# Performance work log

Measured on AMD Instinct MI355X. Metric: run time of the kernel, lower is better.

## Reference

```python
import jax, jax.numpy as jnp
import numpy as np

L, B, D_MODEL, N_STATE = 512, 32, 256, 16
DT_RANK = 16          # ceil(d_model / 16)
D_INNER = D_MODEL     # EXPAND = 1 (required for code self-consistency)


def setup_inputs() -> dict:
    key = jax.random.key(0)
    ks = jax.random.split(key, 6)
    return {
        "position_features": jax.random.normal(ks[0], (L, B, D_MODEL), jnp.float32),
        "flow_features": jax.random.normal(ks[1], (L, B, D_MODEL), jnp.float32),
        "h_state": jnp.zeros((B, D_INNER, N_STATE), jnp.float32),
        "x_proj_w": jax.random.normal(ks[2], (DT_RANK + 2 * N_STATE, D_INNER), jnp.float32) / np.sqrt(D_INNER).astype(np.float32),
        "dt_proj_w": jax.random.normal(ks[3], (D_INNER, DT_RANK), jnp.float32) / np.sqrt(DT_RANK).astype(np.float32),
        "dt_proj_b": jax.random.normal(ks[4], (D_INNER,), jnp.float32) * 0.01,
        "A_log": jnp.log(jnp.broadcast_to(jnp.arange(1, N_STATE + 1, dtype=jnp.float32), (D_INNER, N_STATE))),
        "D_param": jnp.ones((D_INNER,), jnp.float32),
        "out_proj_w": jax.random.normal(ks[5], (D_MODEL, D_INNER), jnp.float32) / np.sqrt(D_INNER).astype(np.float32),
    }


def _forward(position_features, flow_features, h_state,
             x_proj_w, dt_proj_w, dt_proj_b, A_log, D_param, out_proj_w):
    # permute (L, B, d) -> (B, L, d), matching forward()'s permute(1,0,2)
    u = jnp.transpose(position_features, (1, 0, 2))      # (b, l, d_in)
    flow = jnp.transpose(flow_features, (1, 0, 2))       # (b, l, d_in)

    # input-dependent delta, B, C from flow features
    x_dbl = flow @ x_proj_w.T                            # (b, l, dt_rank + 2n)
    delta, Bm, Cm = jnp.split(x_dbl, [DT_RANK, DT_RANK + N_STATE], axis=-1)
    delta = jax.nn.softplus(delta @ dt_proj_w.T + dt_proj_b)   # (b, l, d_in)

    A = -jnp.exp(A_log)                                  # (d_in, n)
    deltaA = jnp.exp(jnp.einsum('bld,dn->bldn', delta, A))         # (b,l,d,n)
    deltaB_u = jnp.einsum('bld,bln,bld->bldn', delta, Bm, u)       # (b,l,d,n)

    # sequential selective scan over l via lax.scan
    dA_t = jnp.swapaxes(deltaA, 0, 1)                    # (l, b, d, n)
    dBu_t = jnp.swapaxes(deltaB_u, 0, 1)                 # (l, b, d, n)
    C_t = jnp.swapaxes(Cm, 0, 1)                         # (l, b, n)

    def step(h, xs):
        dA, dBu, c = xs
        h = dA * h + dBu                                 # (b, d, n)
        y = jnp.einsum('bdn,bn->bd', h, c)               # (b, d)
        return h, y

    h_final, ys = jax.lax.scan(step, h_state, (dA_t, dBu_t, C_t))
    y = jnp.swapaxes(ys, 0, 1)                           # (b, l, d_in)
    y = y + u * D_param                                  # skip connection

    out = y @ out_proj_w.T                               # (b, l, d_model)
    return out.reshape(out.shape[0], -1), h_final        # flatten(1)


def reference(position_features, flow_features, h_state,
              x_proj_w, dt_proj_w, dt_proj_b, A_log, D_param, out_proj_w):
    return _forward(position_features, flow_features, h_state,
                    x_proj_w, dt_proj_w, dt_proj_b, A_log, D_param, out_proj_w)
```

## Files before the change

### kernel.cpp

```cpp
#include <hip/hip_runtime.h>
#include <hip/hip_bf16.h>

#define LL 512
#define BB 32
#define DD 256
#define NS 16
#define RK 16
#define CH3 16
#define LC3 32
#define DT3 32

typedef __attribute__((ext_vector_type(8))) short bf16x8;
typedef __attribute__((ext_vector_type(4))) float f32x4;

#define LD16(dst, src, off) { \
  float4 _v0 = *reinterpret_cast<const float4*>(&(src)[(off)]); \
  float4 _v1 = *reinterpret_cast<const float4*>(&(src)[(off)+4]); \
  float4 _v2 = *reinterpret_cast<const float4*>(&(src)[(off)+8]); \
  float4 _v3 = *reinterpret_cast<const float4*>(&(src)[(off)+12]); \
  dst[0]=_v0.x; dst[1]=_v0.y; dst[2]=_v0.z; dst[3]=_v0.w; \
  dst[4]=_v1.x; dst[5]=_v1.y; dst[6]=_v1.z; dst[7]=_v1.w; \
  dst[8]=_v2.x; dst[9]=_v2.y; dst[10]=_v2.z; dst[11]=_v2.w; \
  dst[12]=_v3.x; dst[13]=_v3.y; dst[14]=_v3.z; dst[15]=_v3.w; }

static __device__ __forceinline__ unsigned short f2bf(float x) {
    __hip_bfloat16 h = __float2bfloat16(x);
    return *reinterpret_cast<unsigned short*>(&h);
}

__global__ __launch_bounds__(256) void k0_wbf(
    const float* __restrict__ W, unsigned short* __restrict__ Wbf)
{
    int i = (blockIdx.x * 256 + threadIdx.x) * 4;
    float4 v = *reinterpret_cast<const float4*>(&W[i]);
    ushort4 o;
    o.x = f2bf(v.x); o.y = f2bf(v.y); o.z = f2bf(v.z); o.w = f2bf(v.w);
    *reinterpret_cast<ushort4*>(&Wbf[i]) = o;
}

__global__ __launch_bounds__(256) void k1_proj(
    const float* __restrict__ flow,
    const float* __restrict__ x_proj_w,
    const float* __restrict__ dt_w,
    const float* __restrict__ dt_b,
    float* __restrict__ delta,
    float* __restrict__ Bm,
    float* __restrict__ Cm)
{
    const int ROWS = 32;
    const int FP = 260;
    const int SP = 49;
    __shared__ float sW[24 * FP];
    __shared__ float sflow[ROWS * FP];
    __shared__ float sdbl[ROWS * SP];
    int tid = threadIdx.x;
    int row0 = blockIdx.x * ROWS;

    #pragma unroll
    for (int jj = 0; jj < 8; ++jj) {
        int s = tid + jj * 256;
        int r = s >> 6, c4 = s & 63;
        int row = row0 + r;
        int b = row >> 9, l = row & 511;
        float4 v = *reinterpret_cast<const float4*>(&flow[(l * BB + b) * DD + c4 * 4]);
        *reinterpret_cast<float4*>(&sflow[r * FP + c4 * 4]) = v;
    }

    int r = tid >> 3, cg = tid & 7;
    const float* frow = &sflow[r * FP];

    for (int half = 0; half < 2; ++half) {
        if (half) __syncthreads();
        #pragma unroll
        for (int jj = 0; jj < 6; ++jj) {
            int s = tid + jj * 256;
            int c = s >> 6, c4 = s & 63;
            float4 v = *reinterpret_cast<const float4*>(&x_proj_w[(half * 24 + c) * DD + c4 * 4]);
            *reinterpret_cast<float4*>(&sW[c * FP + c4 * 4]) = v;
        }
        __syncthreads();

        float acc3[3] = {};
        const float* w0 = &sW[(cg * 3 + 0) * FP];
        const float* w1 = &sW[(cg * 3 + 1) * FP];
        const float* w2 = &sW[(cg * 3 + 2) * FP];
        for (int k = 0; k < DD; k += 4) {
            float4 fv = *reinterpret_cast<const float4*>(&frow[k]);
            float4 wv0 = *reinterpret_cast<const float4*>(&w0[k]);
            float4 wv1 = *reinterpret_cast<const float4*>(&w1[k]);
            float4 wv2 = *reinterpret_cast<const float4*>(&w2[k]);
            acc3[0] = fmaf(fv.x, wv0.x, acc3[0]); acc3[0] = fmaf(fv.y, wv0.y, acc3[0]);
            acc3[0] = fmaf(fv.z, wv0.z, acc3[0]); acc3[0] = fmaf(fv.w, wv0.w, acc3[0]);
            acc3[1] = fmaf(fv.x, wv1.x, acc3[1]); acc3[1] = fmaf(fv.y, wv1.y, acc3[1]);
            acc3[1] = fmaf(fv.z, wv1.z, acc3[1]); acc3[1] = fmaf(fv.w, wv1.w, acc3[1]);
            acc3[2] = fmaf(fv.x, wv2.x, acc3[2]); acc3[2] = fmaf(fv.y, wv2.y, acc3[2]);
            acc3[2] = fmaf(fv.z, wv2.z, acc3[2]); acc3[2] = fmaf(fv.w, wv2.w, acc3[2]);
        }
        #pragma unroll
        for (int j = 0; j < 3; ++j) sdbl[r * SP + half * 24 + cg * 3 + j] = acc3[j];
    }
    __syncthreads();

    #pragma unroll
    for (int jj = 0; jj < 2; ++jj) {
        int idx = tid + jj * 256;
        int rr = idx >> 4, c = idx & 15;
        Bm[(row0 + rr) * NS + c] = sdbl[rr * SP + RK + c];
        Cm[(row0 + rr) * NS + c] = sdbl[rr * SP + RK + NS + c];
    }

    float wreg[RK];
    #pragma unroll
    for (int k = 0; k < RK; k += 4) {
        float4 v = *reinterpret_cast<const float4*>(&dt_w[tid * RK + k]);
        wreg[k] = v.x; wreg[k + 1] = v.y; wreg[k + 2] = v.z; wreg[k + 3] = v.w;
    }
    float bias = dt_b[tid];
    for (int rr = 0; rr < ROWS; ++rr) {
        const float* srow = &sdbl[rr * SP];
        float s = bias;
        #pragma unroll
        for (int k = 0; k < RK; ++k) s = fmaf(srow[k], wreg[k], s);
        float sp = fmaxf(s, 0.f) + log1pf(__expf(-fabsf(s)));
        delta[(size_t)(row0 + rr) * DD + tid] = sp;
    }
}

__global__ __launch_bounds__(512) void k2_fused(
    const float* __restrict__ u_pos,
    const float* __restrict__ h0,
    const float* __restrict__ A_log,
    const float* __restrict__ Dp,
    const float* __restrict__ delta,
    const float* __restrict__ Bm,
    const float* __restrict__ Cm,
    unsigned short* __restrict__ ybf,
    float* __restrict__ h_out)
{
    extern __shared__ float smem[];
    float* lap = smem;
    float* lhp = smem + NS * CH3 * DT3;

    int tid = threadIdx.x;
    int b  = blockIdx.x >> 3;
    int dt = blockIdx.x & 7;
    int dl = tid & 31, c = tid >> 5;
    int d  = dt * DT3 + dl;
    int l0 = c * LC3;

    float a[NS];
    #pragma unroll
    for (int n = 0; n < NS; n += 4) {
        float4 v = *reinterpret_cast<const float4*>(&A_log[d * NS + n]);
        a[n]     = -__expf(v.x) * 1.44269504f;
        a[n + 1] = -__expf(v.y) * 1.44269504f;
        a[n + 2] = -__expf(v.z) * 1.44269504f;
        a[n + 3] = -__expf(v.w) * 1.44269504f;
    }

    const float* dp = delta + ((size_t)b * LL + l0) * DD + d;
    const float* up = u_pos + ((size_t)l0 * BB + b) * DD + d;
    const float* Bp = Bm + ((size_t)b * LL + l0) * NS;
    const float* Cp = Cm + ((size_t)b * LL + l0) * NS;

    float h[NS], ap[NS];
    #pragma unroll
    for (int n = 0; n < NS; ++n) { h[n] = 0.f; ap[n] = 1.f; }

    for (int l = 0; l < LC3; l += 2) {
        float d0 = dp[l * DD],        d1 = dp[(l + 1) * DD];
        float u0 = up[l * BB * DD],   u1 = up[(l + 1) * BB * DD];
        float B0[NS], B1[NS];
        LD16(B0, Bp, l * NS);
        LD16(B1, Bp, (l + 1) * NS);
        float du0 = d0 * u0, du1 = d1 * u1;
        #pragma unroll
        for (int n = 0; n < NS; ++n) {
            float dA = exp2f(d0 * a[n]);
            ap[n] *= dA;
            h[n] = fmaf(dA, h[n], du0 * B0[n]);
        }
        #pragma unroll
        for (int n = 0; n < NS; ++n) {
            float dA = exp2f(d1 * a[n]);
            ap[n] *= dA;
            h[n] = fmaf(dA, h[n], du1 * B1[n]);
        }
    }
    #pragma unroll
    for (int n = 0; n < NS; ++n) {
        lap[n * (CH3 * DT3) + c * DT3 + dl] = ap[n];
        lhp[n * (CH3 * DT3) + c * DT3 + dl] = h[n];
    }
    __syncthreads();

    {
        int dl2 = tid & 31, n2 = tid >> 5;
        float s = h0[((size_t)b * DD + dt * DT3 + dl2) * NS + n2];
        #pragma unroll 4
        for (int c2 = 0; c2 < CH3; ++c2) {
            int idx = n2 * (CH3 * DT3) + c2 * DT3 + dl2;
            float apv = lap[idx];
            float hpv = lhp[idx];
            lap[idx] = s;
            s = fmaf(apv, s, hpv);
        }
        h_out[((size_t)b * DD + dt * DT3 + dl2) * NS + n2] = s;
    }
    __syncthreads();

    #pragma unroll
    for (int n = 0; n < NS; ++n)
        h[n] = lap[n * (CH3 * DT3) + c * DT3 + dl];
    float Dd = Dp[d];
    unsigned short* yp = ybf + ((size_t)b * LL + l0) * DD + d;

    for (int l = 0; l < LC3; l += 2) {
        float d0 = dp[l * DD],        d1 = dp[(l + 1) * DD];
        float u0 = up[l * BB * DD],   u1 = up[(l + 1) * BB * DD];
        float B0[NS], B1[NS], C0[NS], C1[NS];
        LD16(B0, Bp, l * NS);
        LD16(B1, Bp, (l + 1) * NS);
        LD16(C0, Cp, l * NS);
        LD16(C1, Cp, (l + 1) * NS);

        float du0 = d0 * u0, du1 = d1 * u1;
        float acc0 = 0.f, acc1 = 0.f;
        #pragma unroll
        for (int n = 0; n < NS; ++n) {
            float dA = exp2f(d0 * a[n]);
            h[n] = fmaf(dA, h[n], du0 * B0[n]);
            acc0 = fmaf(h[n], C0[n], acc0);
        }
        #pragma unroll
        for (int n = 0; n < NS; ++n) {
            float dA = exp2f(d1 * a[n]);
            h[n] = fmaf(dA, h[n], du1 * B1[n]);
            acc1 = fmaf(h[n], C1[n], acc1);
        }
        yp[l * DD]       = f2bf(fmaf(u0, Dd, acc0));
        yp[(l + 1) * DD] = f2bf(fmaf(u1, Dd, acc1));
    }
}

__global__ __launch_bounds__(256) void k3_mfma(
    const unsigned short* __restrict__ Ybf,
    const unsigned short* __restrict__ Wbf,
    float* __restrict__ Out)
{
    int wave = threadIdx.x >> 6;
    int lane = threadIdx.x & 63;
    int row0 = (blockIdx.x >> 1) * 64 + (wave >> 1) * 32;
    int col0 = (blockIdx.x & 1) * 128 + (wave & 1) * 64;
    int rl = lane & 15, kb = lane >> 4;

    f32x4 acc[2][4] = {};
    bf16x8 af[2], bf[4], afn[2], bfn[4];

    #pragma unroll
    for (int i = 0; i < 2; ++i)
        af[i] = *reinterpret_cast<const bf16x8*>(&Ybf[(size_t)(row0 + i * 16 + rl) * DD + kb * 8]);
    #pragma unroll
    for (int j = 0; j < 4; ++j)
        bf[j] = *reinterpret_cast<const bf16x8*>(&Wbf[(size_t)(col0 + j * 16 + rl) * DD + kb * 8]);

    #pragma unroll
    for (int ks = 0; ks < 8; ++ks) {
        int kn = (ks + 1) * 32 + kb * 8;
        if (ks < 7) {
            #pragma unroll
            for (int i = 0; i < 2; ++i)
                afn[i] = *reinterpret_cast<const bf16x8*>(&Ybf[(size_t)(row0 + i * 16 + rl) * DD + kn]);
            #pragma unroll
            for (int j = 0; j < 4; ++j)
                bfn[j] = *reinterpret_cast<const bf16x8*>(&Wbf[(size_t)(col0 + j * 16 + rl) * DD + kn]);
        }
        #pragma unroll
        for (int i = 0; i < 2; ++i)
            #pragma unroll
            for (int j = 0; j < 4; ++j)
                acc[i][j] = __builtin_amdgcn_mfma_f32_16x16x32_bf16(af[i], bf[j], acc[i][j], 0, 0, 0);
        #pragma unroll
        for (int i = 0; i < 2; ++i) af[i] = afn[i];
        #pragma unroll
        for (int j = 0; j < 4; ++j) bf[j] = bfn[j];
    }

    #pragma unroll
    for (int i = 0; i < 2; ++i)
        #pragma unroll
        for (int j = 0; j < 4; ++j)
            #pragma unroll
            for (int reg = 0; reg < 4; ++reg)
                Out[(size_t)(row0 + i * 16 + kb * 4 + reg) * DD + col0 + j * 16 + rl] = acc[i][j][reg];
}

extern "C" void kernel_launch(void* const* d_in, const int* in_sizes, int n_in,
                              void* d_out, int out_size, void* d_ws, size_t ws_size,
                              hipStream_t stream) {
    const float* pos  = (const float*)d_in[0];
    const float* flow = (const float*)d_in[1];
    const float* h0   = (const float*)d_in[2];
    const float* xw   = (const float*)d_in[3];
    const float* dtw  = (const float*)d_in[4];
    const float* dtb  = (const float*)d_in[5];
    const float* alog = (const float*)d_in[6];
    const float* dpar = (const float*)d_in[7];
    const float* ow   = (const float*)d_in[8];

    float* out = (float*)d_out;

    float* ws    = (float*)d_ws;
    float* delta = ws;
    float* Bmw   = ws + 4194304;
    float* Cmw   = ws + 4456448;
    unsigned short* ybf = (unsigned short*)(ws + 4718592);
    unsigned short* wbf = (unsigned short*)(ws + 6815744);

    float* h_out = out + 32 * 512 * 256;

    k0_wbf  <<<64,  256, 0, stream>>>(ow, wbf);
    k1_proj <<<512, 256, 0, stream>>>(flow, xw, dtw, dtb, delta, Bmw, Cmw);
    k2_fused<<<256, 512, 65536, stream>>>(pos, h0, alog, dpar, delta, Bmw, Cmw, ybf, h_out);
    k3_mfma <<<512, 256, 0, stream>>>(ybf, wbf, out);
}
```

Before: 181.4 us.

## Use f16 MFMA for x_proj GEMM and retile scan into more blocks

Splits the projection kernel in two. The first computes flow @ x_proj_w^T with f16 MFMA instructions, converting fp32 inputs on load, and writes an intermediate xdbl buffer. The second does the small dt projection and softplus from that buffer. The scan kernel is retiled to 16 d-channels × 32 chunks of 16 steps per block, doubling the grid to 512 blocks for better occupancy across CUs. The trade-offs are f16 rounding in the x_proj result, an extra launch and global round trip, and only half the threads doing the inter-chunk combine, which now walks twice as many chunks.

```diff
diff --git a/kernel.cpp b/kernel.cpp
--- a/kernel.cpp
+++ b/kernel.cpp
@@ -6,11 +6,12 @@
 #define DD 256
 #define NS 16
 #define RK 16
-#define CH3 16
-#define LC3 32
-#define DT3 32
+#define CH4 32
+#define LC4 16
+#define DT4 16
 
 typedef __attribute__((ext_vector_type(8))) short bf16x8;
+typedef __attribute__((ext_vector_type(8))) _Float16 f16x8;
 typedef __attribute__((ext_vector_type(4))) float f32x4;
 
 #define LD16(dst, src, off) { \
@@ -28,6 +29,15 @@
     return *reinterpret_cast<unsigned short*>(&h);
 }
 
+static __device__ __forceinline__ f16x8 ld_cvt_f16(const float* p) {
+    float4 lo = *reinterpret_cast<const float4*>(p);
+    float4 hi = *reinterpret_cast<const float4*>(p + 4);
+    f16x8 r;
+    r[0] = (_Float16)lo.x; r[1] = (_Float16)lo.y; r[2] = (_Float16)lo.z; r[3] = (_Float16)lo.w;
+    r[4] = (_Float16)hi.x; r[5] = (_Float16)hi.y; r[6] = (_Float16)hi.z; r[7] = (_Float16)hi.w;
+    return r;
+}
+
 __global__ __launch_bounds__(256) void k0_wbf(
     const float* __restrict__ W, unsigned short* __restrict__ Wbf)
 {
@@ -38,75 +48,66 @@
     *reinterpret_cast<ushort4*>(&Wbf[i]) = o;
 }
 
-__global__ __launch_bounds__(256) void k1_proj(
+__global__ __launch_bounds__(256) void k1a_xdbl(
     const float* __restrict__ flow,
     const float* __restrict__ x_proj_w,
+    float* __restrict__ xdbl)
+{
+    int wave = threadIdx.x >> 6;
+    int lane = threadIdx.x & 63;
+    int rl = lane & 15, kb = lane >> 4;
+    int arow = blockIdx.x * 64 + wave * 16 + rl;
+    int b = arow >> 9, l = arow & 511;
+    const float* abase = &flow[(l * BB + b) * DD];
+
+    f32x4 acc[3] = {};
+    #pragma unroll
+    for (int ks = 0; ks < 8; ++ks) {
+        int k0 = ks * 32 + kb * 8;
+        f16x8 af = ld_cvt_f16(abase + k0);
+        #pragma unroll
+        for (int j = 0; j < 3; ++j) {
+            f16x8 bf = ld_cvt_f16(&x_proj_w[(j * 16 + rl) * DD + k0]);
+            acc[j] = __builtin_amdgcn_mfma_f32_16x16x32_f16(af, bf, acc[j], 0, 0, 0);
+        }
+    }
+    int row_out = blockIdx.x * 64 + wave * 16 + kb * 4;
+    #pragma unroll
+    for (int j = 0; j < 3; ++j)
+        #pragma unroll
+        for (int reg = 0; reg < 4; ++reg)
+            xdbl[(size_t)(row_out + reg) * 48 + j * 16 + rl] = acc[j][reg];
+}
+
+__global__ __launch_bounds__(256) void k1b_proj(
+    const float* __restrict__ xdbl,
     const float* __restrict__ dt_w,
     const float* __restrict__ dt_b,
     float* __restrict__ delta,
     float* __restrict__ Bm,
     float* __restrict__ Cm)
 {
-    const int ROWS = 32;
-    const int FP = 260;
-    const int SP = 49;
-    __shared__ float sW[24 * FP];
-    __shared__ float sflow[ROWS * FP];
-    __shared__ float sdbl[ROWS * SP];
+    __shared__ float sx[32 * 48];
     int tid = threadIdx.x;
-    int row0 = blockIdx.x * ROWS;
-
-    #pragma unroll
-    for (int jj = 0; jj < 8; ++jj) {
-        int s = tid + jj * 256;
-        int r = s >> 6, c4 = s & 63;
-        int row = row0 + r;
-        int b = row >> 9, l = row & 511;
-        float4 v = *reinterpret_cast<const float4*>(&flow[(l * BB + b) * DD + c4 * 4]);
-        *reinterpret_cast<float4*>(&sflow[r * FP + c4 * 4]) = v;
-    }
-
-    int r = tid >> 3, cg = tid & 7;
-    const float* frow = &sflow[r * FP];
-
-    for (int half = 0; half < 2; ++half) {
-        if (half) __syncthreads();
-        #pragma unroll
-        for (int jj = 0; jj < 6; ++jj) {
-            int s = tid + jj * 256;
-            int c = s >> 6, c4 = s & 63;
-            float4 v = *reinterpret_cast<const float4*>(&x_proj_w[(half * 24 + c) * DD + c4 * 4]);
-            *reinterpret_cast<float4*>(&sW[c * FP + c4 * 4]) = v;
-        }
-        __syncthreads();
-
-        float acc3[3] = {};
-        const float* w0 = &sW[(cg * 3 + 0) * FP];
-        const float* w1 = &sW[(cg * 3 + 1) * FP];
-        const float* w2 = &sW[(cg * 3 + 2) * FP];
-        for (int k = 0; k < DD; k += 4) {
-            float4 fv = *reinterpret_cast<const float4*>(&frow[k]);
-            float4 wv0 = *reinterpret_cast<const float4*>(&w0[k]);
-            float4 wv1 = *reinterpret_cast<const float4*>(&w1[k]);
-            float4 wv2 = *reinterpret_cast<const float4*>(&w2[k]);
-            acc3[0] = fmaf(fv.x, wv0.x, acc3[0]); acc3[0] = fmaf(fv.y, wv0.y, acc3[0]);
-            acc3[0] = fmaf(fv.z, wv0.z, acc3[0]); acc3[0] = fmaf(fv.w, wv0.w, acc3[0]);
-            acc3[1] = fmaf(fv.x, wv1.x, acc3[1]); acc3[1] = fmaf(fv.y, wv1.y, acc3[1]);
-            acc3[1] = fmaf(fv.z, wv1.z, acc3[1]); acc3[1] = fmaf(fv.w, wv1.w, acc3[1]);
-            acc3[2] = fmaf(fv.x, wv2.x, acc3[2]); acc3[2] = fmaf(fv.y, wv2.y, acc3[2]);
-            acc3[2] = fmaf(fv.z, wv2.z, acc3[2]); acc3[2] = fmaf(fv.w, wv2.w, acc3[2]);
-        }
-        #pragma unroll
-        for (int j = 0; j < 3; ++j) sdbl[r * SP + half * 24 + cg * 3 + j] = acc3[j];
+    int row0 = blockIdx.x * 32;
+
+    {
+        int i4 = tid;
+        *reinterpret_cast<float4*>(&sx[i4 * 4]) =
+            *reinterpret_cast<const float4*>(&xdbl[(size_t)row0 * 48 + i4 * 4]);
+        i4 = tid + 256;
+        if (i4 < 384)
+            *reinterpret_cast<float4*>(&sx[i4 * 4]) =
+                *reinterpret_cast<const float4*>(&xdbl[(size_t)row0 * 48 + i4 * 4]);
     }
     __syncthreads();
 
     #pragma unroll
     for (int jj = 0; jj < 2; ++jj) {
         int idx = tid + jj * 256;
-        int rr = idx >> 4, c = idx & 15;
-        Bm[(row0 + rr) * NS + c] = sdbl[rr * SP + RK + c];
-        Cm[(row0 + rr) * NS + c] = sdbl[rr * SP + RK + NS + c];
+        int r = idx >> 4, c = idx & 15;
+        Bm[(size_t)(row0 + r) * NS + c] = sx[r * 48 + RK + c];
+        Cm[(size_t)(row0 + r) * NS + c] = sx[r * 48 + RK + NS + c];
     }
 
     float wreg[RK];
@@ -116,13 +117,13 @@
         wreg[k] = v.x; wreg[k + 1] = v.y; wreg[k + 2] = v.z; wreg[k + 3] = v.w;
     }
     float bias = dt_b[tid];
-    for (int rr = 0; rr < ROWS; ++rr) {
-        const float* srow = &sdbl[rr * SP];
+    for (int r = 0; r < 32; ++r) {
+        const float* srow = &sx[r * 48];
         float s = bias;
         #pragma unroll
         for (int k = 0; k < RK; ++k) s = fmaf(srow[k], wreg[k], s);
         float sp = fmaxf(s, 0.f) + log1pf(__expf(-fabsf(s)));
-        delta[(size_t)(row0 + rr) * DD + tid] = sp;
+        delta[(size_t)(row0 + r) * DD + tid] = sp;
     }
 }
 
@@ -139,14 +140,14 @@
 {
     extern __shared__ float smem[];
     float* lap = smem;
-    float* lhp = smem + NS * CH3 * DT3;
+    float* lhp = smem + NS * CH4 * DT4;
 
     int tid = threadIdx.x;
-    int b  = blockIdx.x >> 3;
-    int dt = blockIdx.x & 7;
-    int dl = tid & 31, c = tid >> 5;
-    int d  = dt * DT3 + dl;
-    int l0 = c * LC3;
+    int b  = blockIdx.x >> 4;
+    int dt = blockIdx.x & 15;
+    int dl = tid & 15, c = tid >> 4;
+    int d  = dt * DT4 + dl;
+    int l0 = c * LC4;
 
     float a[NS];
     #pragma unroll
@@ -167,7 +168,7 @@
     #pragma unroll
     for (int n = 0; n < NS; ++n) { h[n] = 0.f; ap[n] = 1.f; }
 
-    for (int l = 0; l < LC3; l += 2) {
+    for (int l = 0; l < LC4; l += 2) {
         float d0 = dp[l * DD],        d1 = dp[(l + 1) * DD];
         float u0 = up[l * BB * DD],   u1 = up[(l + 1) * BB * DD];
         float B0[NS], B1[NS];
@@ -189,33 +190,33 @@
     }
     #pragma unroll
     for (int n = 0; n < NS; ++n) {
-        lap[n * (CH3 * DT3) + c * DT3 + dl] = ap[n];
-        lhp[n * (CH3 * DT3) + c * DT3 + dl] = h[n];
+        lap[n * (CH4 * DT4) + c * DT4 + dl] = ap[n];
+        lhp[n * (CH4 * DT4) + c * DT4 + dl] = h[n];
     }
     __syncthreads();
 
-    {
-        int dl2 = tid & 31, n2 = tid >> 5;
-        float s = h0[((size_t)b * DD + dt * DT3 + dl2) * NS + n2];
+    if (tid < DT4 * NS) {
+        int dl2 = tid & 15, n2 = tid >> 4;
+        float s = h0[((size_t)b * DD + dt * DT4 + dl2) * NS + n2];
         #pragma unroll 4
-        for (int c2 = 0; c2 < CH3; ++c2) {
-            int idx = n2 * (CH3 * DT3) + c2 * DT3 + dl2;
+        for (int c2 = 0; c2 < CH4; ++c2) {
+            int idx = n2 * (CH4 * DT4) + c2 * DT4 + dl2;
             float apv = lap[idx];
             float hpv = lhp[idx];
             lap[idx] = s;
             s = fmaf(apv, s, hpv);
         }
-        h_out[((size_t)b * DD + dt * DT3 + dl2) * NS + n2] = s;
+        h_out[((size_t)b * DD + dt * DT4 + dl2) * NS + n2] = s;
     }
     __syncthreads();
 
     #pragma unroll
     for (int n = 0; n < NS; ++n)
-        h[n] = lap[n * (CH3 * DT3) + c * DT3 + dl];
+        h[n] = lap[n * (CH4 * DT4) + c * DT4 + dl];
     float Dd = Dp[d];
     unsigned short* yp = ybf + ((size_t)b * LL + l0) * DD + d;
 
-    for (int l = 0; l < LC3; l += 2) {
+    for (int l = 0; l < LC4; l += 2) {
         float d0 = dp[l * DD],        d1 = dp[(l + 1) * DD];
         float u0 = up[l * BB * DD],   u1 = up[(l + 1) * BB * DD];
         float B0[NS], B1[NS], C0[NS], C1[NS];
@@ -316,11 +317,13 @@
     float* Cmw   = ws + 4456448;
     unsigned short* ybf = (unsigned short*)(ws + 4718592);
     unsigned short* wbf = (unsigned short*)(ws + 6815744);
+    float* xdbl  = ws + 6848512;
 
     float* h_out = out + 32 * 512 * 256;
 
     k0_wbf  <<<64,  256, 0, stream>>>(ow, wbf);
-    k1_proj <<<512, 256, 0, stream>>>(flow, xw, dtw, dtb, delta, Bmw, Cmw);
-    k2_fused<<<256, 512, 65536, stream>>>(pos, h0, alog, dpar, delta, Bmw, Cmw, ybf, h_out);
+    k1a_xdbl<<<256, 256, 0, stream>>>(flow, xw, xdbl);
+    k1b_proj<<<512, 256, 0, stream>>>(xdbl, dtw, dtb, delta, Bmw, Cmw);
+    k2_fused<<<512, 512, 65536, stream>>>(pos, h0, alog, dpar, delta, Bmw, Cmw, ybf, h_out);
     k3_mfma <<<512, 256, 0, stream>>>(ybf, wbf, out);
 }
```

Measured after the change: 184.7 us. No clear change (+1.9%).
